# Kernel tuning notes

Measured on AMD Instinct MI355X. Metric: run time of the kernel, lower is better.

Reference implementation:

```python
import jax, jax.numpy as jnp
import numpy as np

B, S, D = 4, 2048, 1152
H, KVH, HD = 16, 4, 64
SW = 1792
NEG = jnp.float32(-1e9)


def setup_inputs() -> dict:
    key = jax.random.key(0)
    ks = jax.random.split(key, 6)
    x = jax.random.normal(ks[0], (B, S, D), jnp.float32)
    s = 0.02
    wq = jax.random.normal(ks[1], (H * HD, D), jnp.float32) * s
    wk = jax.random.normal(ks[2], (KVH * HD, D), jnp.float32) * s
    wv = jax.random.normal(ks[3], (KVH * HD, D), jnp.float32) * s
    wo = jax.random.normal(ks[4], (D, H * HD), jnp.float32) * s
    # rotary freqs: theta=10000, standard llama-style
    inv = 1.0 / (10000.0 ** (np.arange(0, HD, 2, dtype=np.float32) / HD))
    t = np.arange(S, dtype=np.float32)
    fr = np.outer(t, inv)  # [S, HD//2]
    freqs_cos = jnp.asarray(np.cos(fr), jnp.float32)
    freqs_sin = jnp.asarray(np.sin(fr), jnp.float32)
    positions = jnp.arange(S, dtype=jnp.int32)
    # sliding-window causal additive mask: attend j iff 0 <= i-j < SW
    i = jnp.arange(S)[:, None]
    j = jnp.arange(S)[None, :]
    allowed = (j <= i) & (i - j < SW)
    mask = jnp.where(allowed, jnp.float32(0.0), NEG)
    cache_k = jnp.zeros((B, SW, KVH, HD), jnp.float32)
    cache_v = jnp.zeros((B, SW, KVH, HD), jnp.float32)
    return {"x": x, "wq": wq, "wk": wk, "wv": wv, "wo": wo,
            "freqs_cos": freqs_cos, "freqs_sin": freqs_sin, "mask": mask,
            "cache_k": cache_k, "cache_v": cache_v, "positions": positions}


def _rope(t, cos, sin):
    # t: [B,S,h,HD]; complex multiply on (even, odd) pairs
    tr = t.reshape(t.shape[:-1] + (HD // 2, 2))
    a, b = tr[..., 0], tr[..., 1]
    c = cos[None, :, None, :]
    s = sin[None, :, None, :]
    out = jnp.stack([a * c - b * s, a * s + b * c], axis=-1)
    return out.reshape(t.shape)


def reference(x, wq, wk, wv, wo, freqs_cos, freqs_sin, mask, cache_k, cache_v, positions):
    bsz, seqlen, _ = x.shape
    xq = jnp.einsum('bsd,ed->bse', x, wq).reshape(bsz, seqlen, H, HD)
    xk = jnp.einsum('bsd,ed->bse', x, wk).reshape(bsz, seqlen, KVH, HD)
    xv = jnp.einsum('bsd,ed->bse', x, wv).reshape(bsz, seqlen, KVH, HD)
    xq = _rope(xq, freqs_cos, freqs_sin)
    xk = _rope(xk, freqs_cos, freqs_sin)
    # circular-buffer cache scatter (last SW tokens, modulo indexing)
    idx = positions[-SW:] % SW
    new_ck = cache_k.at[:, idx].set(xk[:, -SW:])
    new_cv = cache_v.at[:, idx].set(xv[:, -SW:])
    # GQA: expand kv heads (repeat_interleave on head dim)
    rep = H // KVH
    key = jnp.repeat(xk, rep, axis=2)   # [B,S,H,HD]
    value = jnp.repeat(xv, rep, axis=2)
    q = xq.transpose(0, 2, 1, 3)        # [B,H,S,HD]
    k = key.transpose(0, 2, 1, 3)
    v = value.transpose(0, 2, 1, 3)
    scale = 1.0 / jnp.sqrt(jnp.float32(HD))
    scores = jnp.einsum('bhqd,bhkd->bhqk', q, k) * scale + mask[None, None]
    probs = jax.nn.softmax(scores, axis=-1)
    out = jnp.einsum('bhqk,bhkd->bhqd', probs, v)
    out = out.transpose(0, 2, 1, 3).reshape(bsz, seqlen, H * HD)
    out = jnp.einsum('bse,de->bsd', out, wo)
    return out, new_ck, new_cv
```

## Files before the change

kernel.cpp:

```cpp
#include <hip/hip_runtime.h>
#include <cstdint>
#include <cstddef>


typedef unsigned short u16;
typedef unsigned int   u32;
typedef __attribute__((ext_vector_type(8))) short bf16x8;
typedef __attribute__((ext_vector_type(4))) float f32x4;

#define AS1(p) ((const __attribute__((address_space(1))) void*)(p))
#define AS3(p) ((__attribute__((address_space(3))) void*)(p))

__device__ __forceinline__ u16 f2bf(float f) {
  u32 u = __float_as_uint(f);
  u += 0x7fffu + ((u >> 16) & 1u);
  return (u16)(u >> 16);
}
__device__ __forceinline__ float bf2f(u32 x) { return __uint_as_float(x << 16); }
__device__ __forceinline__ f32x4 mfma16(bf16x8 a, bf16x8 b, f32x4 c) {
  return __builtin_amdgcn_mfma_f32_16x16x32_bf16(a, b, c, 0, 0, 0);
}
__device__ __forceinline__ u32 cvtpk_bf16(float lo, float hi) {
  u32 r;
  asm("v_cvt_pk_bf16_f32 %0, %1, %2" : "=v"(r) : "v"(lo), "v"(hi));
  return r;
}

__global__ __launch_bounds__(256) void cvt5_kernel(const float* __restrict__ x,
                                                   const float* __restrict__ wq,
                                                   const float* __restrict__ wk,
                                                   const float* __restrict__ wv,
                                                   const float* __restrict__ wo,
                                                   u16* __restrict__ xb,
                                                   u16* __restrict__ wqkvb,
                                                   u16* __restrict__ wob) {
  int i = blockIdx.x * 256 + threadIdx.x;
  const float* in; u16* out; int off;
  if (i < 2359296)      { in = x;  out = xb;                  off = i; }
  else if (i < 2654208) { in = wq; out = wqkvb;               off = i - 2359296; }
  else if (i < 2727936) { in = wk; out = wqkvb + 1024 * 1152; off = i - 2654208; }
  else if (i < 2801664) { in = wv; out = wqkvb + 1280 * 1152; off = i - 2727936; }
  else                  { in = wo; out = wob;                 off = i - 2801664; }
  float4 v = ((const float4*)in)[off];
  uint2 o;
  o.x = (u32)f2bf(v.x) | ((u32)f2bf(v.y) << 16);
  o.y = (u32)f2bf(v.z) | ((u32)f2bf(v.w) << 16);
  ((uint2*)out)[off] = o;
}

template<int BF16_OUT>
__global__ __launch_bounds__(256) void gemm_bt(const u16* __restrict__ A,
                                               const u16* __restrict__ B,
                                               void* __restrict__ C,
                                               int M, int N, int K) {
  __shared__ u16 As[128][64];
  __shared__ u16 Bs[128][64];
  const int tid  = threadIdx.x;
  const int w    = tid >> 6, lane = tid & 63;
  const int l15  = lane & 15, hi4 = lane >> 4;
  const int m0   = blockIdx.y * 128, n0 = blockIdx.x * 128;
  const int wr   = w >> 1, wc = w & 1;

  const int srow = lane >> 3;
  const int scol = ((lane & 7) ^ srow) << 3;
  const u16* Ab = A + (size_t)(m0 + w * 32 + srow) * K + scol;
  const u16* Bb = B + (size_t)(n0 + w * 32 + srow) * K + scol;
  u16* AsDst = &As[w * 32][0];
  u16* BsDst = &Bs[w * 32][0];

  const int swz = (l15 & 7) << 4;
  const int c0  = (((hi4 * 16)      ^ swz) >> 1);
  const int c1  = (((64 + hi4 * 16) ^ swz) >> 1);
  const u16* aRd = &As[wr * 64 + l15][0];
  const u16* bRd = &Bs[wc * 64 + l15][0];

  f32x4 acc[4][4] = {};

  for (int kk = 0; kk < K; kk += 64) {
#pragma unroll
    for (int q = 0; q < 4; q++) {
      __builtin_amdgcn_global_load_lds(AS1(Ab + kk + (size_t)q * 8 * K),
                                       AS3(AsDst + q * 8 * 64), 16, 0, 0);
      __builtin_amdgcn_global_load_lds(AS1(Bb + kk + (size_t)q * 8 * K),
                                       AS3(BsDst + q * 8 * 64), 16, 0, 0);
    }
    __syncthreads();
#pragma unroll
    for (int ks = 0; ks < 2; ks++) {
      const int cc = ks ? c1 : c0;
      bf16x8 af[4], bfr[4];
#pragma unroll
      for (int t = 0; t < 4; t++) af[t]  = *(const bf16x8*)(aRd + t * 16 * 64 + cc);
#pragma unroll
      for (int t = 0; t < 4; t++) bfr[t] = *(const bf16x8*)(bRd + t * 16 * 64 + cc);
#pragma unroll
      for (int mi = 0; mi < 4; mi++)
#pragma unroll
        for (int ni = 0; ni < 4; ni++)
          acc[mi][ni] = mfma16(af[mi], bfr[ni], acc[mi][ni]);
    }
    __syncthreads();
  }

#pragma unroll
  for (int mi = 0; mi < 4; mi++) {
#pragma unroll
    for (int r = 0; r < 4; r++) {
      int row = m0 + wr * 64 + mi * 16 + hi4 * 4 + r;
      size_t base = (size_t)row * N + n0 + wc * 64 + l15;
#pragma unroll
      for (int ni = 0; ni < 4; ni++) {
        float v = acc[mi][ni][r];
        if (BF16_OUT) ((u16*)C)[base + ni * 16] = f2bf(v);
        else          ((float*)C)[base + ni * 16] = v;
      }
    }
  }
}

template<int PAIRS, int COLOFF, bool QSCALE>
__global__ __launch_bounds__(256) void rope_kernel(u16* __restrict__ buf,
                                                   float* __restrict__ cache,
                                                   const float* __restrict__ cosT,
                                                   const float* __restrict__ sinT) {
  int idx = blockIdx.x * 256 + threadIdx.x;
  int m = idx / PAIRS, p = idx % PAIRS;
  int s = m & 2047, b = m >> 11;
  int hh = p & 31;
  u32* bp = (u32*)buf + (size_t)m * 768 + COLOFF + p;
  u32 pk = *bp;
  float a  = bf2f(pk & 0xffffu), bb = bf2f(pk >> 16);
  float c  = cosT[s * 32 + hh],  sn = sinT[s * 32 + hh];
  float o0 = a * c - bb * sn;
  float o1 = a * sn + bb * c;
  const float qs = QSCALE ? 0.18033688011112042f : 1.0f;
  *bp = (u32)f2bf(o0 * qs) | ((u32)f2bf(o1 * qs) << 16);
  if (!QSCALE && s >= 256) {
    int pc = (s < 1792) ? s : s - 1792;
    float2* cp = (float2*)(cache + (size_t)(b * 1792 + pc) * 256 + 2 * p);
    *cp = make_float2(o0, o1);
  }
}

__global__ __launch_bounds__(256) void vfuse_kernel(const u16* __restrict__ qkv,
                                                    u16* __restrict__ vT,
                                                    float* __restrict__ ncv) {
  __shared__ u16 tile[64][65];
  int s0 = blockIdx.x * 64, kvh = blockIdx.y, b = blockIdx.z;
  int t = threadIdx.x;
  int r = t >> 2, cc = (t & 3) * 16;
  const u16* src = qkv + (size_t)(b * 2048 + s0 + r) * 1536 + 1280 + kvh * 64 + cc;
  uint4 v0 = *(const uint4*)src;
  uint4 v1 = *(const uint4*)(src + 8);
  u16 vals[16];
  *(uint4*)&vals[0] = v0;
  *(uint4*)&vals[8] = v1;
  int s = s0 + r;
  if (s >= 256) {
    int pc = (s < 1792) ? s : s - 1792;
    float* dst = ncv + (size_t)(b * 1792 + pc) * 256 + kvh * 64 + cc;
#pragma unroll
    for (int i = 0; i < 16; i += 4) {
      float4 f = make_float4(bf2f(vals[i]), bf2f(vals[i + 1]),
                             bf2f(vals[i + 2]), bf2f(vals[i + 3]));
      *(float4*)(dst + i) = f;
    }
  }
#pragma unroll
  for (int i = 0; i < 16; i++) tile[cc + i][r] = vals[i];
  __syncthreads();
  u16 ov[16];
#pragma unroll
  for (int i = 0; i < 16; i++) ov[i] = tile[r][cc + i];
  u16* dst2 = vT + (size_t)((b * 4 + kvh) * 64 + r) * 2048 + s0 + cc;
  *(uint4*)dst2 = *(uint4*)&ov[0];
  *(uint4*)(dst2 + 8) = *(uint4*)&ov[8];
}

__global__ __launch_bounds__(256) void attn_kernel(const u16* __restrict__ qkv,
                                                   const u16* __restrict__ vT,
                                                   u16* __restrict__ attnb) {
  __shared__ __align__(16) u16 Kbuf[2][64][64];
  __shared__ __align__(16) u16 Vbuf[2][64][64];
  const int tid = threadIdx.x;
  const int w = tid >> 6, lane = tid & 63;
  const int l15 = lane & 15, hi4 = lane >> 4;

  const int lid  = blockIdx.x + 64 * (blockIdx.y + 4 * blockIdx.z);
  const int wgid = (lid & 7) * 128 + (lid >> 3);
  const int gx   = wgid & 63;
  const int rr   = wgid >> 6;
  const int kvh  = rr & 3, b = rr >> 2;
  const int i0   = 32 * (63 - gx);
  const int h    = kvh * 4 + w;

  const u16* qbase = qkv + (size_t)(b * 2048) * 1536 + h * 64;
  const u16* kbase = qkv + (size_t)(b * 2048) * 1536 + 1024 + kvh * 64;
  const u16* vbase = vT + (size_t)((b * 4 + kvh) * 64) * 2048;

  bf16x8 qa[2][2];
  {
    const u16* qp = qbase + (size_t)(i0 + l15) * 1536 + hi4 * 8;
#pragma unroll
    for (int m = 0; m < 2; m++)
#pragma unroll
      for (int ki = 0; ki < 2; ki++)
        qa[m][ki] = *(const bf16x8*)(qp + m * 16 * 1536 + ki * 32);
  }

  bf16x8 ones;
#pragma unroll
  for (int i = 0; i < 8; i++) ones[i] = (short)0x3F80;

  f32x4 o[2][4] = {};
  f32x4 ol[2] = {};

  const int srow = lane >> 3;
  const int ssl  = (lane & 7) ^ srow;

#define STAGE(J0, BS)                                                                     \
  do {                                                                                    \
    _Pragma("unroll")                                                                     \
    for (int q = 0; q < 2; q++) {                                                         \
      const int row = 32 * q + 8 * w + srow;                                              \
      __builtin_amdgcn_global_load_lds(AS1(kbase + (size_t)((J0) + row) * 1536 + ssl * 8),\
                                       AS3(&Kbuf[BS][32 * q + 8 * w][0]), 16, 0, 0);      \
      __builtin_amdgcn_global_load_lds(AS1(vbase + (size_t)row * 2048 + (J0) + ssl * 8),  \
                                       AS3(&Vbuf[BS][32 * q + 8 * w][0]), 16, 0, 0);      \
    }                                                                                     \
  } while (0)

  int jstart = i0 - 1791;
  if (jstart < 0) jstart = 0;
  jstart &= ~63;
  const int jend = i0 + 32;
  const int ntiles = (jend - jstart + 63) >> 6;

  STAGE(jstart, 0);
  if (ntiles > 1) STAGE(jstart + 64, 1);

  for (int t = 0; t < ntiles; t++) {
    const int j0 = jstart + 64 * t;
    if (t + 1 < ntiles) asm volatile("s_waitcnt vmcnt(4)" ::: "memory");
    else                asm volatile("s_waitcnt vmcnt(0)" ::: "memory");
    __builtin_amdgcn_s_barrier();
    __builtin_amdgcn_sched_barrier(0);

    const u16* Kb = &Kbuf[t & 1][0][0];
    const u16* Vb = &Vbuf[t & 1][0][0];

    bf16x8 kf[2][4];
#pragma unroll
    for (int nt = 0; nt < 4; nt++)
#pragma unroll
      for (int ki = 0; ki < 2; ki++)
        kf[ki][nt] = *(const bf16x8*)(Kb + (nt * 16 + l15) * 64 +
                                      (((ki * 4 + hi4) ^ (l15 & 7)) << 3));

    u32 vfd[4][2][4];
#pragma unroll
    for (int tt = 0; tt < 4; tt++) {
      const int row = tt * 16 + l15;
      const u16* Vrow = Vb + row * 64;
      const int rs = row & 7;
      const int inner = (hi4 & 1) * 4;
      const int h1 = hi4 >> 1;
#pragma unroll
      for (int kbp = 0; kbp < 2; kbp++) {
        int us0 = (((4 * kbp + h1)     ^ rs) << 3) + inner;
        int us1 = (((4 * kbp + 2 + h1) ^ rs) << 3) + inner;
        uint2 lo = *(const uint2*)(Vrow + us0);
        uint2 hi = *(const uint2*)(Vrow + us1);
        vfd[tt][kbp][0] = lo.x; vfd[tt][kbp][1] = lo.y;
        vfd[tt][kbp][2] = hi.x; vfd[tt][kbp][3] = hi.y;
      }
    }
    asm volatile("s_waitcnt lgkmcnt(0)" ::: "memory");
    __builtin_amdgcn_sched_barrier(0);
    __builtin_amdgcn_s_barrier();
    if (t + 2 < ntiles) STAGE(j0 + 128, t & 1);

    __builtin_amdgcn_s_setprio(1);
    const bool fast = (j0 + 63 <= i0) && (i0 + 31 - j0 < 1792);
#pragma unroll
    for (int m = 0; m < 2; m++) {
      __align__(16) u32 pkb[8];
#pragma unroll
      for (int nt = 0; nt < 4; nt++) {
        f32x4 s = {0.f, 0.f, 0.f, 0.f};
        s = mfma16(kf[0][nt], qa[m][0], s);
        s = mfma16(kf[1][nt], qa[m][1], s);
        float p[4];
        if (fast) {
#pragma unroll
          for (int r = 0; r < 4; r++) p[r] = __builtin_amdgcn_exp2f(s[r]);
        } else {
#pragma unroll
          for (int r = 0; r < 4; r++) {
            const int j = j0 + nt * 16 + hi4 * 4 + r;
            const int i = i0 + m * 16 + l15;
            p[r] = (j <= i && i - j < 1792) ? __builtin_amdgcn_exp2f(s[r]) : 0.f;
          }
        }
        pkb[nt * 2]     = cvtpk_bf16(p[0], p[1]);
        pkb[nt * 2 + 1] = cvtpk_bf16(p[2], p[3]);
      }
      bf16x8 pa0 = *(const bf16x8*)&pkb[0];
      bf16x8 pa1 = *(const bf16x8*)&pkb[4];
#pragma unroll
      for (int tt = 0; tt < 4; tt++) {
        o[m][tt] = mfma16(pa0, *(const bf16x8*)&vfd[tt][0][0], o[m][tt]);
        o[m][tt] = mfma16(pa1, *(const bf16x8*)&vfd[tt][1][0], o[m][tt]);
      }
      ol[m] = mfma16(pa0, ones, ol[m]);
      ol[m] = mfma16(pa1, ones, ol[m]);
    }
    __builtin_amdgcn_s_setprio(0);
  }
#undef STAGE

  u16* op = attnb + (size_t)(b * 2048 + i0 + hi4 * 4) * 1024 + h * 64 + l15;
#pragma unroll
  for (int m = 0; m < 2; m++)
#pragma unroll
    for (int r = 0; r < 4; r++) {
      float inv = 1.0f / ol[m][r];
#pragma unroll
      for (int tt = 0; tt < 4; tt++)
        op[(size_t)(m * 16 + r) * 1024 + 16 * tt] = f2bf(o[m][tt][r] * inv);
    }
}

extern "C" void kernel_launch(void* const* d_in, const int* in_sizes, int n_in,
                              void* d_out, int out_size, void* d_ws, size_t ws_size,
                              hipStream_t stream) {
  const float* x  = (const float*)d_in[0];
  const float* wq = (const float*)d_in[1];
  const float* wk = (const float*)d_in[2];
  const float* wv = (const float*)d_in[3];
  const float* wo = (const float*)d_in[4];
  const float* fc = (const float*)d_in[5];
  const float* fs = (const float*)d_in[6];

  float* out = (float*)d_out;
  float* nck = out + 9437184;
  float* ncv = nck + 1835008;

  char* ws = (char*)d_ws;
  u16* xb    = (u16*)(ws);
  u16* wqkvb = (u16*)(ws + 18874368);
  u16* wob   = (u16*)(ws + 22413312);
  u16* qkv   = (u16*)(ws + 24772608);
  u16* vT    = (u16*)(ws + 49938432);
  u16* attnb = (u16*)(ws + 54132736);

  cvt5_kernel<<<12096, 256, 0, stream>>>(x, wq, wk, wv, wo, xb, wqkvb, wob);

  gemm_bt<1><<<dim3(12, 64), 256, 0, stream>>>(xb, wqkvb, qkv, 8192, 1536, 1152);

  rope_kernel<512, 0,   true ><<<16384, 256, 0, stream>>>(qkv, nullptr, fc, fs);
  rope_kernel<128, 512, false><<<4096,  256, 0, stream>>>(qkv, nck, fc, fs);

  vfuse_kernel<<<dim3(32, 4, 4), 256, 0, stream>>>(qkv, vT, ncv);

  attn_kernel<<<dim3(64, 4, 4), 256, 0, stream>>>(qkv, vT, attnb);

  gemm_bt<0><<<dim3(9, 64), 256, 0, stream>>>(attnb, wob, out, 8192, 1152, 1024);
}
```

Baseline: 167.4 us.

## Split long attention rows into KV chunks with atomic reduction; fuse rope launches

Splits the attention work for query blocks with long KV ranges into up to four chunks of 8 tiles. Each chunk accumulates its unnormalized output and row sums into fp32 buffers with atomicAdd, and a new finalize kernel normalizes them and writes bf16. This targets load imbalance and tail effects from the triangular causal workload, at the cost of a memset, fp32 atomic traffic and an extra kernel. The two rope launches are also merged into one kernel, and attnb now aliases the xb workspace.

```diff
diff --git a/kernel.cpp b/kernel.cpp
--- a/kernel.cpp
+++ b/kernel.cpp
@@ -118,24 +118,27 @@
   }
 }
 
-template<int PAIRS, int COLOFF, bool QSCALE>
-__global__ __launch_bounds__(256) void rope_kernel(u16* __restrict__ buf,
-                                                   float* __restrict__ cache,
-                                                   const float* __restrict__ cosT,
-                                                   const float* __restrict__ sinT) {
+__global__ __launch_bounds__(256) void rope_fused(u16* __restrict__ buf,
+                                                  float* __restrict__ cache,
+                                                  const float* __restrict__ cosT,
+                                                  const float* __restrict__ sinT) {
   int idx = blockIdx.x * 256 + threadIdx.x;
-  int m = idx / PAIRS, p = idx % PAIRS;
+  const bool isQ = idx < 4194304;
+  int pi = isQ ? idx : idx - 4194304;
+  int m  = isQ ? (pi >> 9) : (pi >> 7);
+  int p  = isQ ? (pi & 511) : (pi & 127);
+  int coloff = isQ ? 0 : 512;
   int s = m & 2047, b = m >> 11;
   int hh = p & 31;
-  u32* bp = (u32*)buf + (size_t)m * 768 + COLOFF + p;
+  u32* bp = (u32*)buf + (size_t)m * 768 + coloff + p;
   u32 pk = *bp;
   float a  = bf2f(pk & 0xffffu), bb = bf2f(pk >> 16);
   float c  = cosT[s * 32 + hh],  sn = sinT[s * 32 + hh];
   float o0 = a * c - bb * sn;
   float o1 = a * sn + bb * c;
-  const float qs = QSCALE ? 0.18033688011112042f : 1.0f;
+  const float qs = isQ ? 0.18033688011112042f : 1.0f;
   *bp = (u32)f2bf(o0 * qs) | ((u32)f2bf(o1 * qs) << 16);
-  if (!QSCALE && s >= 256) {
+  if (!isQ && s >= 256) {
     int pc = (s < 1792) ? s : s - 1792;
     float2* cp = (float2*)(cache + (size_t)(b * 1792 + pc) * 256 + 2 * p);
     *cp = make_float2(o0, o1);
@@ -179,20 +182,28 @@
 
 __global__ __launch_bounds__(256) void attn_kernel(const u16* __restrict__ qkv,
                                                    const u16* __restrict__ vT,
-                                                   u16* __restrict__ attnb) {
+                                                   u16* __restrict__ attnb,
+                                                   float* __restrict__ Of,
+                                                   float* __restrict__ lf) {
   __shared__ __align__(16) u16 Kbuf[2][64][64];
   __shared__ __align__(16) u16 Vbuf[2][64][64];
   const int tid = threadIdx.x;
   const int w = tid >> 6, lane = tid & 63;
   const int l15 = lane & 15, hi4 = lane >> 4;
 
-  const int lid  = blockIdx.x + 64 * (blockIdx.y + 4 * blockIdx.z);
-  const int wgid = (lid & 7) * 128 + (lid >> 3);
-  const int gx   = wgid & 63;
-  const int rr   = wgid >> 6;
+  const int lid  = blockIdx.x + 160 * (blockIdx.y + 4 * blockIdx.z);
+  const int wgid = (lid & 7) * 320 + (lid >> 3);
+  const int xs   = 159 - (wgid % 160);
+  const int rr   = wgid / 160;
   const int kvh  = rr & 3, b = rr >> 2;
-  const int i0   = 32 * (63 - gx);
-  const int h    = kvh * 4 + w;
+  int c, ch, nch;
+  if (xs < 16)      { c = xs;                      ch = 0;            nch = 1; }
+  else if (xs < 48) { int t2 = xs - 16; c = 16 + (t2 >> 1); ch = t2 & 1; nch = 2; }
+  else if (xs < 96) { int t2 = xs - 48; c = 32 + t2 / 3;    ch = t2 % 3; nch = 3; }
+  else              { int t2 = xs - 96; c = 48 + (t2 >> 2); ch = t2 & 3; nch = 4; }
+  const int i0 = 32 * c;
+  const int T  = (c >= 56) ? 29 : ((c + 2) >> 1);
+  const int h  = kvh * 4 + w;
 
   const u16* qbase = qkv + (size_t)(b * 2048) * 1536 + h * 64;
   const u16* kbase = qkv + (size_t)(b * 2048) * 1536 + 1024 + kvh * 64;
@@ -230,19 +241,19 @@
     }                                                                                     \
   } while (0)
 
-  int jstart = i0 - 1791;
-  if (jstart < 0) jstart = 0;
-  jstart &= ~63;
-  const int jend = i0 + 32;
-  const int ntiles = (jend - jstart + 63) >> 6;
+  int jf = i0 - 1791;
+  if (jf < 0) jf = 0;
+  jf &= ~63;
+  const int jstart = jf + 512 * ch;
+  int ntc = T - 8 * ch; if (ntc > 8) ntc = 8;
 
   STAGE(jstart, 0);
-  if (ntiles > 1) STAGE(jstart + 64, 1);
-
-  for (int t = 0; t < ntiles; t++) {
+  if (ntc > 1) STAGE(jstart + 64, 1);
+
+  for (int t = 0; t < ntc; t++) {
     const int j0 = jstart + 64 * t;
-    if (t + 1 < ntiles) asm volatile("s_waitcnt vmcnt(4)" ::: "memory");
-    else                asm volatile("s_waitcnt vmcnt(0)" ::: "memory");
+    if (t + 1 < ntc) asm volatile("s_waitcnt vmcnt(4)" ::: "memory");
+    else             asm volatile("s_waitcnt vmcnt(0)" ::: "memory");
     __builtin_amdgcn_s_barrier();
     __builtin_amdgcn_sched_barrier(0);
 
@@ -278,7 +289,7 @@
     asm volatile("s_waitcnt lgkmcnt(0)" ::: "memory");
     __builtin_amdgcn_sched_barrier(0);
     __builtin_amdgcn_s_barrier();
-    if (t + 2 < ntiles) STAGE(j0 + 128, t & 1);
+    if (t + 2 < ntc) STAGE(j0 + 128, t & 1);
 
     __builtin_amdgcn_s_setprio(1);
     const bool fast = (j0 + 63 <= i0) && (i0 + 31 - j0 < 1792);
@@ -319,16 +330,51 @@
   }
 #undef STAGE
 
-  u16* op = attnb + (size_t)(b * 2048 + i0 + hi4 * 4) * 1024 + h * 64 + l15;
-#pragma unroll
-  for (int m = 0; m < 2; m++)
-#pragma unroll
-    for (int r = 0; r < 4; r++) {
-      float inv = 1.0f / ol[m][r];
-#pragma unroll
-      for (int tt = 0; tt < 4; tt++)
-        op[(size_t)(m * 16 + r) * 1024 + 16 * tt] = f2bf(o[m][tt][r] * inv);
-    }
+  if (nch == 1) {
+    u16* op = attnb + (size_t)(b * 2048 + i0 + hi4 * 4) * 1024 + h * 64 + l15;
+#pragma unroll
+    for (int m = 0; m < 2; m++)
+#pragma unroll
+      for (int r = 0; r < 4; r++) {
+        float inv = 1.0f / ol[m][r];
+#pragma unroll
+        for (int tt = 0; tt < 4; tt++)
+          op[(size_t)(m * 16 + r) * 1024 + 16 * tt] = f2bf(o[m][tt][r] * inv);
+      }
+  } else {
+    float* Ob = Of + (size_t)(b * 1536 + (i0 - 512) + hi4 * 4) * 1024 + h * 64 + l15;
+#pragma unroll
+    for (int m = 0; m < 2; m++)
+#pragma unroll
+      for (int r = 0; r < 4; r++) {
+        float* Or = Ob + (size_t)(m * 16 + r) * 1024;
+#pragma unroll
+        for (int tt = 0; tt < 4; tt++) atomicAdd(Or + 16 * tt, o[m][tt][r]);
+      }
+    if (l15 == 0) {
+#pragma unroll
+      for (int m = 0; m < 2; m++)
+#pragma unroll
+        for (int r = 0; r < 4; r++)
+          atomicAdd(lf + (size_t)(b * 1536 + (i0 - 512) + m * 16 + hi4 * 4 + r) * 16 + h,
+                    ol[m][r]);
+    }
+  }
+}
+
+__global__ __launch_bounds__(256) void attn_fin(const float* __restrict__ Of,
+                                                const float* __restrict__ lf,
+                                                u16* __restrict__ attnb) {
+  int idx = blockIdx.x * 256 + threadIdx.x;
+  int col = (idx & 255) * 4;
+  int rowg = idx >> 8;
+  float inv = 1.0f / lf[rowg * 16 + (col >> 6)];
+  float4 v = *(const float4*)(Of + (size_t)rowg * 1024 + col);
+  int b = rowg / 1536, row = rowg % 1536;
+  uint2 o2;
+  o2.x = (u32)f2bf(v.x * inv) | ((u32)f2bf(v.y * inv) << 16);
+  o2.y = (u32)f2bf(v.z * inv) | ((u32)f2bf(v.w * inv) << 16);
+  *(uint2*)(attnb + (size_t)(b * 2048 + 512 + row) * 1024 + col) = o2;
 }
 
 extern "C" void kernel_launch(void* const* d_in, const int* in_sizes, int n_in,
@@ -347,23 +393,28 @@
   float* ncv = nck + 1835008;
 
   char* ws = (char*)d_ws;
-  u16* xb    = (u16*)(ws);
-  u16* wqkvb = (u16*)(ws + 18874368);
-  u16* wob   = (u16*)(ws + 22413312);
-  u16* qkv   = (u16*)(ws + 24772608);
-  u16* vT    = (u16*)(ws + 49938432);
-  u16* attnb = (u16*)(ws + 54132736);
+  u16*   attnb = (u16*)(ws);
+  u16*   xb    = (u16*)(ws);
+  u16*   wqkvb = (u16*)(ws + 18874368);
+  u16*   wob   = (u16*)(ws + 22413312);
+  u16*   qkv   = (u16*)(ws + 24772608);
+  u16*   vT    = (u16*)(ws + 49938432);
+  float* Of    = (float*)(ws + 54132736);
+  float* lf    = (float*)(ws + 79298560);
+
+  hipMemsetAsync(Of, 0, 25165824 + 393216, stream);
 
   cvt5_kernel<<<12096, 256, 0, stream>>>(x, wq, wk, wv, wo, xb, wqkvb, wob);
 
   gemm_bt<1><<<dim3(12, 64), 256, 0, stream>>>(xb, wqkvb, qkv, 8192, 1536, 1152);
 
-  rope_kernel<512, 0,   true ><<<16384, 256, 0, stream>>>(qkv, nullptr, fc, fs);
-  rope_kernel<128, 512, false><<<4096,  256, 0, stream>>>(qkv, nck, fc, fs);
+  rope_fused<<<20480, 256, 0, stream>>>(qkv, nck, fc, fs);
 
   vfuse_kernel<<<dim3(32, 4, 4), 256, 0, stream>>>(qkv, vT, ncv);
 
-  attn_kernel<<<dim3(64, 4, 4), 256, 0, stream>>>(qkv, vT, attnb);
+  attn_kernel<<<dim3(160, 4, 4), 256, 0, stream>>>(qkv, vT, attnb, Of, lf);
+
+  attn_fin<<<6144, 256, 0, stream>>>(Of, lf, attnb);
 
   gemm_bt<0><<<dim3(9, 64), 256, 0, stream>>>(attnb, wob, out, 8192, 1152, 1024);
 }
```

Result: slower. 223.5 us (+33.5%).

## Fuse RoPE and V-transpose kernels, remap attention blocks per XCD, alias workspace

Applied to the files above, without the earlier changes.

Merges the two RoPE launches (Q and K) and the V transpose/cache kernel into one launch that branches on block index, removing two kernel launches and their gaps. The attention grid becomes 1D with a new block-to-work mapping that keeps each (batch, kv-head) pair on one XCD and pairs long and short causal rows for load balance, aiming at better L2 reuse of K/V. The attention output buffer now aliases the dead bf16 x buffer to shrink the workspace footprint. The fused kernel carries a shared-memory tile even for RoPE blocks, which may reduce occupancy for that part.

```diff
diff --git a/kernel.cpp b/kernel.cpp
--- a/kernel.cpp
+++ b/kernel.cpp
@@ -118,63 +118,67 @@
   }
 }
 
-template<int PAIRS, int COLOFF, bool QSCALE>
-__global__ __launch_bounds__(256) void rope_kernel(u16* __restrict__ buf,
-                                                   float* __restrict__ cache,
-                                                   const float* __restrict__ cosT,
-                                                   const float* __restrict__ sinT) {
-  int idx = blockIdx.x * 256 + threadIdx.x;
-  int m = idx / PAIRS, p = idx % PAIRS;
-  int s = m & 2047, b = m >> 11;
-  int hh = p & 31;
-  u32* bp = (u32*)buf + (size_t)m * 768 + COLOFF + p;
-  u32 pk = *bp;
-  float a  = bf2f(pk & 0xffffu), bb = bf2f(pk >> 16);
-  float c  = cosT[s * 32 + hh],  sn = sinT[s * 32 + hh];
-  float o0 = a * c - bb * sn;
-  float o1 = a * sn + bb * c;
-  const float qs = QSCALE ? 0.18033688011112042f : 1.0f;
-  *bp = (u32)f2bf(o0 * qs) | ((u32)f2bf(o1 * qs) << 16);
-  if (!QSCALE && s >= 256) {
-    int pc = (s < 1792) ? s : s - 1792;
-    float2* cp = (float2*)(cache + (size_t)(b * 1792 + pc) * 256 + 2 * p);
-    *cp = make_float2(o0, o1);
-  }
-}
-
-__global__ __launch_bounds__(256) void vfuse_kernel(const u16* __restrict__ qkv,
+__global__ __launch_bounds__(256) void ropev_kernel(u16* __restrict__ buf,
+                                                    float* __restrict__ kcache,
                                                     u16* __restrict__ vT,
-                                                    float* __restrict__ ncv) {
+                                                    float* __restrict__ ncv,
+                                                    const float* __restrict__ cosT,
+                                                    const float* __restrict__ sinT) {
   __shared__ u16 tile[64][65];
-  int s0 = blockIdx.x * 64, kvh = blockIdx.y, b = blockIdx.z;
-  int t = threadIdx.x;
-  int r = t >> 2, cc = (t & 3) * 16;
-  const u16* src = qkv + (size_t)(b * 2048 + s0 + r) * 1536 + 1280 + kvh * 64 + cc;
-  uint4 v0 = *(const uint4*)src;
-  uint4 v1 = *(const uint4*)(src + 8);
-  u16 vals[16];
-  *(uint4*)&vals[0] = v0;
-  *(uint4*)&vals[8] = v1;
-  int s = s0 + r;
-  if (s >= 256) {
-    int pc = (s < 1792) ? s : s - 1792;
-    float* dst = ncv + (size_t)(b * 1792 + pc) * 256 + kvh * 64 + cc;
-#pragma unroll
-    for (int i = 0; i < 16; i += 4) {
-      float4 f = make_float4(bf2f(vals[i]), bf2f(vals[i + 1]),
-                             bf2f(vals[i + 2]), bf2f(vals[i + 3]));
-      *(float4*)(dst + i) = f;
-    }
-  }
-#pragma unroll
-  for (int i = 0; i < 16; i++) tile[cc + i][r] = vals[i];
-  __syncthreads();
-  u16 ov[16];
-#pragma unroll
-  for (int i = 0; i < 16; i++) ov[i] = tile[r][cc + i];
-  u16* dst2 = vT + (size_t)((b * 4 + kvh) * 64 + r) * 2048 + s0 + cc;
-  *(uint4*)dst2 = *(uint4*)&ov[0];
-  *(uint4*)(dst2 + 8) = *(uint4*)&ov[8];
+  if (blockIdx.x < 20480) {
+    int idx = blockIdx.x * 256 + threadIdx.x;
+    const bool isQ = idx < 4194304;
+    int pi = isQ ? idx : idx - 4194304;
+    int m  = isQ ? (pi >> 9) : (pi >> 7);
+    int p  = isQ ? (pi & 511) : (pi & 127);
+    int coloff = isQ ? 0 : 512;
+    int s = m & 2047, b = m >> 11;
+    int hh = p & 31;
+    u32* bp = (u32*)buf + (size_t)m * 768 + coloff + p;
+    u32 pk = *bp;
+    float a  = bf2f(pk & 0xffffu), bb = bf2f(pk >> 16);
+    float c  = cosT[s * 32 + hh],  sn = sinT[s * 32 + hh];
+    float o0 = a * c - bb * sn;
+    float o1 = a * sn + bb * c;
+    const float qs = isQ ? 0.18033688011112042f : 1.0f;
+    *bp = (u32)f2bf(o0 * qs) | ((u32)f2bf(o1 * qs) << 16);
+    if (!isQ && s >= 256) {
+      int pc = (s < 1792) ? s : s - 1792;
+      float2* cp = (float2*)(kcache + (size_t)(b * 1792 + pc) * 256 + 2 * p);
+      *cp = make_float2(o0, o1);
+    }
+  } else {
+    int bi = blockIdx.x - 20480;
+    int s0 = (bi & 31) * 64, kvh = (bi >> 5) & 3, b = bi >> 7;
+    int t = threadIdx.x;
+    int r = t >> 2, cc = (t & 3) * 16;
+    const u16* src = buf + (size_t)(b * 2048 + s0 + r) * 1536 + 1280 + kvh * 64 + cc;
+    uint4 v0 = *(const uint4*)src;
+    uint4 v1 = *(const uint4*)(src + 8);
+    u16 vals[16];
+    *(uint4*)&vals[0] = v0;
+    *(uint4*)&vals[8] = v1;
+    int s = s0 + r;
+    if (s >= 256) {
+      int pc = (s < 1792) ? s : s - 1792;
+      float* dst = ncv + (size_t)(b * 1792 + pc) * 256 + kvh * 64 + cc;
+#pragma unroll
+      for (int i = 0; i < 16; i += 4) {
+        float4 f = make_float4(bf2f(vals[i]), bf2f(vals[i + 1]),
+                               bf2f(vals[i + 2]), bf2f(vals[i + 3]));
+        *(float4*)(dst + i) = f;
+      }
+    }
+#pragma unroll
+    for (int i = 0; i < 16; i++) tile[cc + i][r] = vals[i];
+    __syncthreads();
+    u16 ov[16];
+#pragma unroll
+    for (int i = 0; i < 16; i++) ov[i] = tile[r][cc + i];
+    u16* dst2 = vT + (size_t)((b * 4 + kvh) * 64 + r) * 2048 + s0 + cc;
+    *(uint4*)dst2 = *(uint4*)&ov[0];
+    *(uint4*)(dst2 + 8) = *(uint4*)&ov[8];
+  }
 }
 
 __global__ __launch_bounds__(256) void attn_kernel(const u16* __restrict__ qkv,
@@ -186,13 +190,15 @@
   const int w = tid >> 6, lane = tid & 63;
   const int l15 = lane & 15, hi4 = lane >> 4;
 
-  const int lid  = blockIdx.x + 64 * (blockIdx.y + 4 * blockIdx.z);
-  const int wgid = (lid & 7) * 128 + (lid >> 3);
-  const int gx   = wgid & 63;
-  const int rr   = wgid >> 6;
-  const int kvh  = rr & 3, b = rr >> 2;
-  const int i0   = 32 * (63 - gx);
-  const int h    = kvh * 4 + w;
+  const int lid   = blockIdx.x;
+  const int xcd   = lid & 7;
+  const int t_    = lid >> 3;
+  const int chunk = t_ >> 5, pos = t_ & 31;
+  const int rr    = xcd * 2 + (chunk >> 1);
+  const int kvh   = rr & 3, b = rr >> 2;
+  const int c     = (chunk & 1) ? pos : (63 - pos);
+  const int i0    = 32 * c;
+  const int h     = kvh * 4 + w;
 
   const u16* qbase = qkv + (size_t)(b * 2048) * 1536 + h * 64;
   const u16* kbase = qkv + (size_t)(b * 2048) * 1536 + 1024 + kvh * 64;
@@ -347,23 +353,20 @@
   float* ncv = nck + 1835008;
 
   char* ws = (char*)d_ws;
+  u16* attnb = (u16*)(ws);
   u16* xb    = (u16*)(ws);
   u16* wqkvb = (u16*)(ws + 18874368);
   u16* wob   = (u16*)(ws + 22413312);
   u16* qkv   = (u16*)(ws + 24772608);
   u16* vT    = (u16*)(ws + 49938432);
-  u16* attnb = (u16*)(ws + 54132736);
 
   cvt5_kernel<<<12096, 256, 0, stream>>>(x, wq, wk, wv, wo, xb, wqkvb, wob);
 
   gemm_bt<1><<<dim3(12, 64), 256, 0, stream>>>(xb, wqkvb, qkv, 8192, 1536, 1152);
 
-  rope_kernel<512, 0,   true ><<<16384, 256, 0, stream>>>(qkv, nullptr, fc, fs);
-  rope_kernel<128, 512, false><<<4096,  256, 0, stream>>>(qkv, nck, fc, fs);
-
-  vfuse_kernel<<<dim3(32, 4, 4), 256, 0, stream>>>(qkv, vT, ncv);
-
-  attn_kernel<<<dim3(64, 4, 4), 256, 0, stream>>>(qkv, vT, attnb);
+  ropev_kernel<<<20992, 256, 0, stream>>>(qkv, nck, vT, ncv, fc, fs);
+
+  attn_kernel<<<1024, 256, 0, stream>>>(qkv, vT, attnb);
 
   gemm_bt<0><<<dim3(9, 64), 256, 0, stream>>>(attnb, wob, out, 8192, 1152, 1024);
 }
```

Result: slower. 172.8 us (+3.2%).
